# Kernel tuning notes

Hardware: AMD Instinct MI355X
Metric: run time of the kernel (lower is better)

The kernel has to match this reference:

```python
import jax, jax.numpy as jnp
import numpy as np

B, T, D = 32, 1024, 1024
N, L = 77, 768
H = 8
TED = 2048  # time_embed_dim
EPS = 1e-5


def _ln(x, g, b):
    m = jnp.mean(x, axis=-1, keepdims=True)
    v = jnp.var(x, axis=-1, keepdims=True)
    return (x - m) * jax.lax.rsqrt(v + EPS) * g + b


def setup_inputs() -> dict:
    key = jax.random.key(0)
    ks = jax.random.split(key, 16)
    s = lambda fan_in: 1.0 / np.sqrt(fan_in)
    return {
        "x": jax.random.normal(ks[0], (B, T, D), jnp.float32),
        "xf": jax.random.normal(ks[1], (B, N, L), jnp.float32),
        "emb": jax.random.normal(ks[2], (B, TED), jnp.float32),
        "norm_g": jnp.ones((D,), jnp.float32),
        "norm_b": jnp.zeros((D,), jnp.float32),
        "tnorm_g": jnp.ones((L,), jnp.float32),
        "tnorm_b": jnp.zeros((L,), jnp.float32),
        "Wq": jax.random.normal(ks[3], (D, D), jnp.float32) * s(D),
        "bq": jnp.zeros((D,), jnp.float32),
        "Wk": jax.random.normal(ks[4], (L, D), jnp.float32) * s(L),
        "bk": jnp.zeros((D,), jnp.float32),
        "Wv": jax.random.normal(ks[5], (L, D), jnp.float32) * s(L),
        "bv": jnp.zeros((D,), jnp.float32),
        "emb_W": jax.random.normal(ks[6], (TED, 2 * D), jnp.float32) * s(TED),
        "emb_b": jnp.zeros((2 * D,), jnp.float32),
        "onorm_g": jnp.ones((D,), jnp.float32),
        "onorm_b": jnp.zeros((D,), jnp.float32),
        "Wo": jax.random.normal(ks[7], (D, D), jnp.float32) * s(D),
        "bo": jnp.zeros((D,), jnp.float32),
    }


def reference(x, xf, emb, norm_g, norm_b, tnorm_g, tnorm_b, Wq, bq, Wk, bk, Wv, bv,
              emb_W, emb_b, onorm_g, onorm_b, Wo, bo):
    Bc, Tc, Dc = x.shape
    Nc = xf.shape[1]
    hd = Dc // H
    # projections
    q = _ln(x, norm_g, norm_b) @ Wq + bq                      # [B,T,D]
    xfn = _ln(xf, tnorm_g, tnorm_b)                           # [B,N,L]
    k = (xfn @ Wk + bk).reshape(Bc, Nc, H, hd)                # [B,N,H,hd]
    v = (xfn @ Wv + bv).reshape(Bc, Nc, H, hd)                # [B,N,H,hd]
    q = jax.nn.softmax(q.reshape(Bc, Tc, H, hd), axis=-1)     # softmax over head_dim
    k = jax.nn.softmax(k, axis=1)                             # softmax over N (key tokens)
    # linear-attention: no TxN matrix
    attn = jnp.einsum('bnhd,bnhl->bhdl', k, v)                # [B,H,hd,hd]
    y = jnp.einsum('bthd,bhdl->bthl', q, attn).reshape(Bc, Tc, Dc)
    # StylizationBlock
    emb_out = jax.nn.silu(emb) @ emb_W + emb_b                # [B,2D]
    scale, shift = jnp.split(emb_out[:, None, :], 2, axis=2)  # [B,1,D] each
    h = _ln(y, onorm_g, onorm_b) * (1.0 + scale) + shift
    h = jax.nn.silu(h) @ Wo + bo
    return x + h
```

## Files before the change

kernel.cpp:

```cpp
#include <hip/hip_runtime.h>
#include <hip/hip_bf16.h>
#include <math.h>

namespace {

constexpr int Bc  = 32;
constexpr int Tc  = 1024;
constexpr int Dc  = 1024;
constexpr int Nt  = 77;
constexpr int Lc  = 768;
constexpr int HDc = 128;
constexpr int TEDc = 2048;
constexpr float EPSc = 1e-5f;

typedef __attribute__((ext_vector_type(8))) short bf16x8;
typedef __attribute__((ext_vector_type(8))) unsigned short u16x8;
typedef __attribute__((ext_vector_type(4))) float f32x4;

__device__ __forceinline__ float silu_f(float x) { return x / (1.f + __expf(-x)); }

__device__ __forceinline__ unsigned short f2bf(float f) {
  unsigned u = __float_as_uint(f);
  return (unsigned short)((u + 0x7fffu + ((u >> 16) & 1u)) >> 16);
}
__device__ __forceinline__ float bf2f(unsigned short h) {
  return __uint_as_float(((unsigned)h) << 16);
}

__device__ __forceinline__ void gload16(const void* g, void* l) {
  __builtin_amdgcn_global_load_lds((const __attribute__((address_space(1))) void*)g,
                                   (__attribute__((address_space(3))) void*)l, 16, 0, 0);
}

__device__ __forceinline__ int rowswz(int r) {
  return (((r >> 3) & 1) << 1) | ((r >> 1) & 1);
}

__global__ __launch_bounds__(256) void ln_bf16_kernel(
    const float* __restrict__ src, unsigned short* __restrict__ dst, int cols,
    const float* __restrict__ g, const float* __restrict__ b)
{
  const int row = blockIdx.x;
  const float* p = src + (size_t)row * cols;
  const int c = threadIdx.x * 4;
  float4 v = make_float4(0.f, 0.f, 0.f, 0.f);
  if (c < cols) v = *reinterpret_cast<const float4*>(p + c);
  float s  = v.x + v.y + v.z + v.w;
  float sq = v.x * v.x + v.y * v.y + v.z * v.z + v.w * v.w;
  __shared__ float red[2][4];
  __shared__ float mr[2];
  for (int o = 32; o > 0; o >>= 1) { s += __shfl_down(s, o); sq += __shfl_down(sq, o); }
  const int wid = threadIdx.x >> 6, lane = threadIdx.x & 63;
  if (lane == 0) { red[0][wid] = s; red[1][wid] = sq; }
  __syncthreads();
  if (threadIdx.x == 0) {
    const float S  = red[0][0] + red[0][1] + red[0][2] + red[0][3];
    const float SQ = red[1][0] + red[1][1] + red[1][2] + red[1][3];
    const float mean = S / cols;
    const float var  = SQ / cols - mean * mean;
    mr[0] = mean; mr[1] = rsqrtf(var + EPSc);
  }
  __syncthreads();
  if (c < cols) {
    const float mean = mr[0], rstd = mr[1];
    ushort4 o;
    o.x = f2bf((v.x - mean) * rstd * g[c + 0] + b[c + 0]);
    o.y = f2bf((v.y - mean) * rstd * g[c + 1] + b[c + 1]);
    o.z = f2bf((v.z - mean) * rstd * g[c + 2] + b[c + 2]);
    o.w = f2bf((v.w - mean) * rstd * g[c + 3] + b[c + 3]);
    *reinterpret_cast<ushort4*>(dst + (size_t)row * cols + c) = o;
  }
}

__global__ __launch_bounds__(256) void convT_bf16_kernel(
    const float* __restrict__ W, unsigned short* __restrict__ Wt, int K, int N)
{
  __shared__ float t[32][33];
  const int n0 = blockIdx.x * 32, k0 = blockIdx.y * 32;
  const int tx = threadIdx.x & 31, ty = threadIdx.x >> 5;
  #pragma unroll
  for (int dy = 0; dy < 32; dy += 8)
    t[ty + dy][tx] = W[(size_t)(k0 + ty + dy) * N + n0 + tx];
  __syncthreads();
  #pragma unroll
  for (int dy = 0; dy < 32; dy += 8)
    Wt[(size_t)(n0 + ty + dy) * K + k0 + tx] = f2bf(t[tx][ty + dy]);
}

__global__ __launch_bounds__(256) void convT2_bf16_kernel(
    const float* __restrict__ W0, unsigned short* __restrict__ T0,
    const float* __restrict__ W1, unsigned short* __restrict__ T1, int K, int N)
{
  __shared__ float t[32][33];
  const float* W = blockIdx.z ? W1 : W0;
  unsigned short* Wt = blockIdx.z ? T1 : T0;
  const int n0 = blockIdx.x * 32, k0 = blockIdx.y * 32;
  const int tx = threadIdx.x & 31, ty = threadIdx.x >> 5;
  #pragma unroll
  for (int dy = 0; dy < 32; dy += 8)
    t[ty + dy][tx] = W[(size_t)(k0 + ty + dy) * N + n0 + tx];
  __syncthreads();
  #pragma unroll
  for (int dy = 0; dy < 32; dy += 8)
    Wt[(size_t)(n0 + ty + dy) * K + k0 + tx] = f2bf(t[tx][ty + dy]);
}

template<int EPI>
__global__ __launch_bounds__(512) void gemm2_kernel(
    const unsigned short* __restrict__ A, const unsigned short* __restrict__ Bt,
    const float* __restrict__ bias, const float* __restrict__ bias2, int bsplit,
    void* __restrict__ Cout, int M, int K, int N, const float* __restrict__ xres)
{
  constexpr int LDSE = (EPI == 2) ? 32768 : 24576;
  __shared__ unsigned short lds[LDSE];
  const int tid = threadIdx.x, wid = tid >> 6, lane = tid & 63;
  const int ntx = N >> 7;
  int swz = blockIdx.x;
  const int nwg = gridDim.x;
  if ((nwg & 7) == 0) { const int cpx = nwg >> 3; swz = (swz & 7) * cpx + (swz >> 3); }
  const int bx = swz % ntx, by = swz / ntx;
  const int bm0 = by << 8, bn0 = bx << 7;
  const int wr = wid >> 1, wc = wid & 1, lhi = lane >> 4, llo = lane & 15;

  const int srow = lane >> 2;
  const int scol = (((lane & 3) ^ rowswz(srow)) * 8);
  int ar0 = bm0 + wid * 32 + srow;      if (ar0 >= M) ar0 = M - 1;
  int ar1 = bm0 + wid * 32 + 16 + srow; if (ar1 >= M) ar1 = M - 1;
  const int br = bn0 + wid * 16 + srow;
  const unsigned short* Ag0 = A  + (size_t)ar0 * K + scol;
  const unsigned short* Ag1 = A  + (size_t)ar1 * K + scol;
  const unsigned short* Bg  = Bt + (size_t)br  * K + scol;
  const int alc0 = (wid * 2) * 512, alc1 = (wid * 2 + 1) * 512, blc = wid * 512;
  const int rx = rowswz(llo);
  const int aoff = wr * 2048 + llo * 32 + ((lhi ^ rx) * 8);
  const int boff = wc * 2048 + llo * 32 + ((lhi ^ rx) * 8);

  f32x4 acc[4][4] = {};
  const int nt = K >> 5;

  gload16(Ag0, &lds[alc0]);
  gload16(Ag1, &lds[alc1]);
  gload16(Bg,  &lds[16384 + blc]);
  __syncthreads();

  int cur = 0;
  for (int t = 1; t < nt; ++t) {
    const int nb = cur ^ 1;
    const int k0 = t << 5;
    gload16(Ag0 + k0, &lds[nb * 8192 + alc0]);
    gload16(Ag1 + k0, &lds[nb * 8192 + alc1]);
    gload16(Bg  + k0, &lds[16384 + nb * 4096 + blc]);
    bf16x8 a_[4], b_[4];
    #pragma unroll
    for (int mi = 0; mi < 4; mi++) a_[mi] = *(const bf16x8*)(&lds[cur * 8192 + aoff + mi * 512]);
    #pragma unroll
    for (int ni = 0; ni < 4; ni++) b_[ni] = *(const bf16x8*)(&lds[16384 + cur * 4096 + boff + ni * 512]);
    #pragma unroll
    for (int mi = 0; mi < 4; mi++)
      #pragma unroll
      for (int ni = 0; ni < 4; ni++)
        acc[mi][ni] = __builtin_amdgcn_mfma_f32_16x16x32_bf16(a_[mi], b_[ni], acc[mi][ni], 0, 0, 0);
    __syncthreads();
    cur = nb;
  }
  {
    bf16x8 a_[4], b_[4];
    #pragma unroll
    for (int mi = 0; mi < 4; mi++) a_[mi] = *(const bf16x8*)(&lds[cur * 8192 + aoff + mi * 512]);
    #pragma unroll
    for (int ni = 0; ni < 4; ni++) b_[ni] = *(const bf16x8*)(&lds[16384 + cur * 4096 + boff + ni * 512]);
    #pragma unroll
    for (int mi = 0; mi < 4; mi++)
      #pragma unroll
      for (int ni = 0; ni < 4; ni++)
        acc[mi][ni] = __builtin_amdgcn_mfma_f32_16x16x32_bf16(a_[mi], b_[ni], acc[mi][ni], 0, 0, 0);
  }

  if constexpr (EPI != 2) {
    #pragma unroll
    for (int mi = 0; mi < 4; mi++) {
      #pragma unroll
      for (int ni = 0; ni < 4; ni++) {
        const int col = bn0 + wc * 64 + ni * 16 + llo;
        const float bs = (bsplit > 0 && col >= bsplit) ? bias2[col - bsplit] : bias[col];
        #pragma unroll
        for (int r = 0; r < 4; r++) {
          const int row = bm0 + wr * 64 + mi * 16 + lhi * 4 + r;
          if (row < M) {
            float v = acc[mi][ni][r] + bs;
            if (EPI == 1) v += xres[(size_t)row * N + col];
            ((float*)Cout)[(size_t)row * N + col] = v;
          }
        }
      }
    }
  } else {
    __syncthreads();
    #pragma unroll
    for (int mi = 0; mi < 4; mi++) {
      #pragma unroll
      for (int ni = 0; ni < 4; ni++) {
        const int col = wc * 64 + ni * 16 + llo;
        const float bs = bias[bn0 + col];
        #pragma unroll
        for (int r = 0; r < 4; r++) {
          const int row = wr * 64 + mi * 16 + lhi * 4 + r;
          lds[row * 128 + (col ^ ((row & 7) << 3))] = f2bf(acc[mi][ni][r] + bs);
        }
      }
    }
    __syncthreads();
    const int row = tid >> 1, cb = (tid & 1) * 64;
    const int sw = (row & 7) << 3;
    float mx = -1e30f;
    #pragma unroll
    for (int g = 0; g < 8; g++) {
      u16x8 u = *(const u16x8*)(&lds[row * 128 + ((cb + g * 8) ^ sw)]);
      #pragma unroll
      for (int j = 0; j < 8; j++) mx = fmaxf(mx, bf2f(u[j]));
    }
    mx = fmaxf(mx, __shfl_xor(mx, 1));
    float ssum = 0.f;
    #pragma unroll
    for (int g = 0; g < 8; g++) {
      unsigned short* p = &lds[row * 128 + ((cb + g * 8) ^ sw)];
      u16x8 u = *(const u16x8*)p;
      u16x8 e;
      #pragma unroll
      for (int j = 0; j < 8; j++) {
        float ev = __expf(bf2f(u[j]) - mx);
        ssum += ev;
        e[j] = f2bf(ev);
      }
      *(u16x8*)p = e;
    }
    ssum += __shfl_xor(ssum, 1);
    const float inv = 1.f / ssum;
    unsigned short* Cb = (unsigned short*)Cout;
    #pragma unroll
    for (int g = 0; g < 8; g++) {
      u16x8 u = *(const u16x8*)(&lds[row * 128 + ((cb + g * 8) ^ sw)]);
      u16x8 o;
      #pragma unroll
      for (int j = 0; j < 8; j++) o[j] = f2bf(bf2f(u[j]) * inv);
      *(u16x8*)(&Cb[(size_t)(bm0 + row) * N + bn0 + cb + g * 8]) = o;
    }
  }
}

__global__ void softmax_k_kernel(float* __restrict__ kv) {
  const int idx = blockIdx.x * blockDim.x + threadIdx.x;
  const int b = idx >> 10, d = idx & 1023;
  float* p = kv + (size_t)b * Nt * 2048 + d;
  float m = -1e30f;
  for (int n = 0; n < Nt; n++) m = fmaxf(m, p[(size_t)n * 2048]);
  float s = 0.f;
  for (int n = 0; n < Nt; n++) s += __expf(p[(size_t)n * 2048] - m);
  const float inv = 1.f / s;
  for (int n = 0; n < Nt; n++) p[(size_t)n * 2048] = __expf(p[(size_t)n * 2048] - m) * inv;
}

__global__ __launch_bounds__(256) void attn_einsum_kernel(
    const float* __restrict__ kv, unsigned short* __restrict__ attnT) {
  const int bh = blockIdx.x;
  const int b = bh >> 3, h = bh & 7;
  __shared__ float ks[Nt][HDc];
  __shared__ float vs[Nt][HDc];
  const float* kb = kv + (size_t)b * Nt * 2048 + h * HDc;
  const float* vb = kv + (size_t)b * Nt * 2048 + 1024 + h * HDc;
  for (int i = threadIdx.x; i < Nt * HDc; i += 256) {
    const int n = i >> 7, d = i & 127;
    ks[n][d] = kb[(size_t)n * 2048 + d];
    vs[n][d] = vb[(size_t)n * 2048 + d];
  }
  __syncthreads();
  const int tx = threadIdx.x & 15, ty = threadIdx.x >> 4;
  float acc[8][8] = {};
  for (int n = 0; n < Nt; n++) {
    float a[8], w[8];
    #pragma unroll
    for (int i = 0; i < 8; i++) a[i] = vs[n][ty + 16 * i];
    #pragma unroll
    for (int j = 0; j < 8; j++) w[j] = ks[n][tx + 16 * j];
    #pragma unroll
    for (int i = 0; i < 8; i++)
      #pragma unroll
      for (int j = 0; j < 8; j++)
        acc[i][j] += a[i] * w[j];
  }
  unsigned short* ab = attnT + (size_t)bh * HDc * HDc;
  #pragma unroll
  for (int i = 0; i < 8; i++)
    #pragma unroll
    for (int j = 0; j < 8; j++)
      ab[(size_t)(ty + 16 * i) * HDc + tx + 16 * j] = f2bf(acc[i][j]);
}

__global__ __launch_bounds__(256) void y_mfma_kernel(
    unsigned short* __restrict__ q, const unsigned short* __restrict__ attnT)
{
  __shared__ unsigned short lds[16384];
  const int tid = threadIdx.x, wid = tid >> 6, lane = tid & 63;
  const int bh = blockIdx.y, b = bh >> 3, h = bh & 7;
  const int bm0 = blockIdx.x << 7;
  const int wr = wid >> 1, wc = wid & 1, lhi = lane >> 4, llo = lane & 15;

  unsigned short* Abase = q + ((size_t)b * Tc) * Dc + h * HDc;
  const unsigned short* Btb = attnT + (size_t)bh * HDc * HDc;

  const int srow = lane >> 2;
  const int scol = (((lane & 3) ^ rowswz(srow)) * 8);
  const int ar0 = bm0 + wid * 32 + srow, ar1 = ar0 + 16;
  const int br0 = wid * 32 + srow,       br1 = br0 + 16;
  const unsigned short* Ag0 = Abase + (size_t)ar0 * Dc + scol;
  const unsigned short* Ag1 = Abase + (size_t)ar1 * Dc + scol;
  const unsigned short* Bg0 = Btb + (size_t)br0 * HDc + scol;
  const unsigned short* Bg1 = Btb + (size_t)br1 * HDc + scol;
  const int lc0 = (wid * 2 + 0) * 512, lc1 = (wid * 2 + 1) * 512;
  const int rx = rowswz(llo);
  const int aoff = wr * 2048 + llo * 32 + ((lhi ^ rx) * 8);
  const int boff = wc * 2048 + llo * 32 + ((lhi ^ rx) * 8);

  f32x4 acc[4][4] = {};

  gload16(Ag0, &lds[lc0]);
  gload16(Ag1, &lds[lc1]);
  gload16(Bg0, &lds[8192 + lc0]);
  gload16(Bg1, &lds[8192 + lc1]);
  __syncthreads();

  int cur = 0;
  for (int t = 1; t < 4; ++t) {
    const int nb = cur ^ 1;
    const int k0 = t << 5;
    gload16(Ag0 + k0, &lds[nb * 4096 + lc0]);
    gload16(Ag1 + k0, &lds[nb * 4096 + lc1]);
    gload16(Bg0 + k0, &lds[8192 + nb * 4096 + lc0]);
    gload16(Bg1 + k0, &lds[8192 + nb * 4096 + lc1]);
    bf16x8 a_[4], b_[4];
    #pragma unroll
    for (int mi = 0; mi < 4; mi++) a_[mi] = *(const bf16x8*)(&lds[cur * 4096 + aoff + mi * 512]);
    #pragma unroll
    for (int ni = 0; ni < 4; ni++) b_[ni] = *(const bf16x8*)(&lds[8192 + cur * 4096 + boff + ni * 512]);
    #pragma unroll
    for (int mi = 0; mi < 4; mi++)
      #pragma unroll
      for (int ni = 0; ni < 4; ni++)
        acc[mi][ni] = __builtin_amdgcn_mfma_f32_16x16x32_bf16(a_[mi], b_[ni], acc[mi][ni], 0, 0, 0);
    __syncthreads();
    cur = nb;
  }
  {
    bf16x8 a_[4], b_[4];
    #pragma unroll
    for (int mi = 0; mi < 4; mi++) a_[mi] = *(const bf16x8*)(&lds[cur * 4096 + aoff + mi * 512]);
    #pragma unroll
    for (int ni = 0; ni < 4; ni++) b_[ni] = *(const bf16x8*)(&lds[8192 + cur * 4096 + boff + ni * 512]);
    #pragma unroll
    for (int mi = 0; mi < 4; mi++)
      #pragma unroll
      for (int ni = 0; ni < 4; ni++)
        acc[mi][ni] = __builtin_amdgcn_mfma_f32_16x16x32_bf16(a_[mi], b_[ni], acc[mi][ni], 0, 0, 0);
  }

  __syncthreads();
  #pragma unroll
  for (int mi = 0; mi < 4; mi++) {
    #pragma unroll
    for (int ni = 0; ni < 4; ni++) {
      const int col = wc * 64 + ni * 16 + llo;
      #pragma unroll
      for (int r = 0; r < 4; r++) {
        const int row = wr * 64 + mi * 16 + lhi * 4 + r;
        lds[row * 128 + (col ^ ((row & 7) << 3))] = f2bf(acc[mi][ni][r]);
      }
    }
  }
  __syncthreads();
  const int row = tid >> 1, cb = (tid & 1) * 64;
  const int sw = (row & 7) << 3;
  #pragma unroll
  for (int g = 0; g < 8; g++) {
    u16x8 u = *(const u16x8*)(&lds[row * 128 + ((cb + g * 8) ^ sw)]);
    *(u16x8*)(&Abase[(size_t)(bm0 + row) * Dc + cb + g * 8]) = u;
  }
}

__global__ __launch_bounds__(256) void ln_mod_silu_bf16_kernel(
    unsigned short* __restrict__ y, const float* __restrict__ ss,
    const float* __restrict__ g, const float* __restrict__ bvec) {
  const int row = blockIdx.x;
  const int b = row >> 10;
  unsigned short* p = y + (size_t)row * Dc;
  const int c = threadIdx.x * 4;
  ushort4 u = *reinterpret_cast<const ushort4*>(p + c);
  float vv[4] = {bf2f(u.x), bf2f(u.y), bf2f(u.z), bf2f(u.w)};
  float s  = vv[0] + vv[1] + vv[2] + vv[3];
  float sq = vv[0]*vv[0] + vv[1]*vv[1] + vv[2]*vv[2] + vv[3]*vv[3];
  __shared__ float red[2][4];
  __shared__ float mr[2];
  for (int o = 32; o > 0; o >>= 1) { s += __shfl_down(s, o); sq += __shfl_down(sq, o); }
  const int wid = threadIdx.x >> 6, lane = threadIdx.x & 63;
  if (lane == 0) { red[0][wid] = s; red[1][wid] = sq; }
  __syncthreads();
  if (threadIdx.x == 0) {
    const float S  = red[0][0] + red[0][1] + red[0][2] + red[0][3];
    const float SQ = red[1][0] + red[1][1] + red[1][2] + red[1][3];
    const float mean = S / Dc;
    const float var = SQ / Dc - mean * mean;
    mr[0] = mean; mr[1] = rsqrtf(var + EPSc);
  }
  __syncthreads();
  const float mean = mr[0], rstd = mr[1];
  const float* ssb = ss + (size_t)b * 2 * Dc;
  ushort4 o;
  float t0 = (vv[0] - mean) * rstd * g[c + 0] + bvec[c + 0];
  float t1 = (vv[1] - mean) * rstd * g[c + 1] + bvec[c + 1];
  float t2 = (vv[2] - mean) * rstd * g[c + 2] + bvec[c + 2];
  float t3 = (vv[3] - mean) * rstd * g[c + 3] + bvec[c + 3];
  o.x = f2bf(silu_f(t0 * (1.f + ssb[c + 0]) + ssb[Dc + c + 0]));
  o.y = f2bf(silu_f(t1 * (1.f + ssb[c + 1]) + ssb[Dc + c + 1]));
  o.z = f2bf(silu_f(t2 * (1.f + ssb[c + 2]) + ssb[Dc + c + 2]));
  o.w = f2bf(silu_f(t3 * (1.f + ssb[c + 3]) + ssb[Dc + c + 3]));
  *reinterpret_cast<ushort4*>(p + c) = o;
}

__global__ __launch_bounds__(256) void silu_emb_kernel(
    const float* __restrict__ emb, float* __restrict__ sile) {
  const int i = (blockIdx.x * 256 + threadIdx.x) * 4;
  float4 v = *reinterpret_cast<const float4*>(emb + i);
  v.x = silu_f(v.x); v.y = silu_f(v.y); v.z = silu_f(v.z); v.w = silu_f(v.w);
  *reinterpret_cast<float4*>(sile + i) = v;
}

__global__ __launch_bounds__(256) void emb_part_kernel(
    const float* __restrict__ sile, const float* __restrict__ W,
    float* __restrict__ part) {
  const int split = blockIdx.y;
  const int n = blockIdx.x * 256 + threadIdx.x;
  const int k0 = split * 64;
  const float* se = sile + k0;
  const float* Wp = W + (size_t)k0 * (2 * Dc) + n;
  float acc[32] = {};
  for (int kk = 0; kk < 64; kk++) {
    const float w = Wp[(size_t)kk * (2 * Dc)];
    #pragma unroll
    for (int m = 0; m < 32; m++)
      acc[m] = fmaf(se[m * TEDc + kk], w, acc[m]);
  }
  float* pp = part + (size_t)split * 32 * (2 * Dc) + n;
  #pragma unroll
  for (int m = 0; m < 32; m++) pp[(size_t)m * (2 * Dc)] = acc[m];
}

__global__ __launch_bounds__(256) void emb_reduce_kernel(
    const float* __restrict__ part, const float* __restrict__ bias,
    float* __restrict__ ssb) {
  const int i = blockIdx.x * 256 + threadIdx.x;
  const int n = i & (2 * Dc - 1);
  float s = bias[n];
  #pragma unroll 8
  for (int sp = 0; sp < 32; sp++) s += part[(size_t)sp * 32 * (2 * Dc) + i];
  ssb[i] = s;
}

}

extern "C" void kernel_launch(void* const* d_in, const int* in_sizes, int n_in,
                              void* d_out, int out_size, void* d_ws, size_t ws_size,
                              hipStream_t stream) {
  const float* x       = (const float*)d_in[0];
  const float* xf      = (const float*)d_in[1];
  const float* emb     = (const float*)d_in[2];
  const float* norm_g  = (const float*)d_in[3];
  const float* norm_b  = (const float*)d_in[4];
  const float* tnorm_g = (const float*)d_in[5];
  const float* tnorm_b = (const float*)d_in[6];
  const float* Wq      = (const float*)d_in[7];
  const float* bq      = (const float*)d_in[8];
  const float* Wk      = (const float*)d_in[9];
  const float* bk      = (const float*)d_in[10];
  const float* Wv      = (const float*)d_in[11];
  const float* bv_     = (const float*)d_in[12];
  const float* emb_W   = (const float*)d_in[13];
  const float* emb_b   = (const float*)d_in[14];
  const float* onorm_g = (const float*)d_in[15];
  const float* onorm_b = (const float*)d_in[16];
  const float* Wo      = (const float*)d_in[17];
  const float* bo      = (const float*)d_in[18];
  float* out = (float*)d_out;

  char* ws = (char*)d_ws;
  unsigned short* Ab = (unsigned short*)ws;
  char* R = ws;
  unsigned short* qb   = (unsigned short*)(ws + 67108864);
  unsigned short* Wq_t = (unsigned short*)(ws + 134217728);
  unsigned short* Wk_t = (unsigned short*)(ws + 136314880);
  unsigned short* Wv_t = (unsigned short*)(ws + 137887744);
  unsigned short* Wo_t = (unsigned short*)(ws + 139460608);
  float*          ssb  = (float*)(ws + 141557760);
  float*          sile = (float*)(ws + 141819904);
  float*          part = (float*)(ws + 142082048);
  unsigned short* xfb   = (unsigned short*)(R);
  float*          kv    = (float*)(R + 3784704);
  unsigned short* attnT = (unsigned short*)(R + 23969792);

  const int Mq  = Bc * Tc;
  const int Mkv = Bc * Nt;

  ln_bf16_kernel<<<Mq, 256, 0, stream>>>(x, Ab, Dc, norm_g, norm_b);
  convT_bf16_kernel<<<dim3(Dc / 32, Dc / 32), 256, 0, stream>>>(Wq, Wq_t, Dc, Dc);
  convT2_bf16_kernel<<<dim3(Dc / 32, Lc / 32, 2), 256, 0, stream>>>(Wk, Wk_t, Wv, Wv_t, Lc, Dc);
  convT_bf16_kernel<<<dim3(Dc / 32, Dc / 32), 256, 0, stream>>>(Wo, Wo_t, Dc, Dc);

  gemm2_kernel<2><<<(Dc / 128) * (Mq / 256), 512, 0, stream>>>(
      Ab, Wq_t, bq, nullptr, 0, qb, Mq, Dc, Dc, nullptr);

  ln_bf16_kernel<<<Mkv, 256, 0, stream>>>(xf, xfb, Lc, tnorm_g, tnorm_b);
  gemm2_kernel<0><<<(2048 / 128) * ((Mkv + 255) / 256), 512, 0, stream>>>(
      xfb, Wk_t, bk, bv_, 1024, kv, Mkv, Lc, 2048, nullptr);
  softmax_k_kernel<<<(Bc * Dc) / 256, 256, 0, stream>>>(kv);
  attn_einsum_kernel<<<Bc * 8, 256, 0, stream>>>(kv, attnT);

  silu_emb_kernel<<<(Bc * TEDc) / 1024, 256, 0, stream>>>(emb, sile);
  emb_part_kernel<<<dim3(8, 32), 256, 0, stream>>>(sile, emb_W, part);
  emb_reduce_kernel<<<(Bc * 2 * Dc) / 256, 256, 0, stream>>>(part, emb_b, ssb);

  y_mfma_kernel<<<dim3(Tc / 128, Bc * 8), 256, 0, stream>>>(qb, attnT);
  ln_mod_silu_bf16_kernel<<<Mq, 256, 0, stream>>>(qb, ssb, onorm_g, onorm_b);
  gemm2_kernel<1><<<(Dc / 128) * (Mq / 256), 512, 0, stream>>>(
      qb, Wo_t, bo, nullptr, 0, out, Mq, Dc, Dc, x);
}
```

Before: 481.6 us.

## Enlarge GEMM block tile to 256x256 with 2x4 wave layout

```diff
diff --git a/kernel.cpp b/kernel.cpp
--- a/kernel.cpp
+++ b/kernel.cpp
@@ -106,57 +106,60 @@
 }
 
 template<int EPI>
-__global__ __launch_bounds__(512) void gemm2_kernel(
+__global__ __launch_bounds__(512, 2) void gemm2_kernel(
     const unsigned short* __restrict__ A, const unsigned short* __restrict__ Bt,
     const float* __restrict__ bias, const float* __restrict__ bias2, int bsplit,
     void* __restrict__ Cout, int M, int K, int N, const float* __restrict__ xres)
 {
-  constexpr int LDSE = (EPI == 2) ? 32768 : 24576;
-  __shared__ unsigned short lds[LDSE];
+  __shared__ unsigned short lds[32768];
   const int tid = threadIdx.x, wid = tid >> 6, lane = tid & 63;
-  const int ntx = N >> 7;
+  const int ntx = N >> 8;
   int swz = blockIdx.x;
   const int nwg = gridDim.x;
   if ((nwg & 7) == 0) { const int cpx = nwg >> 3; swz = (swz & 7) * cpx + (swz >> 3); }
   const int bx = swz % ntx, by = swz / ntx;
-  const int bm0 = by << 8, bn0 = bx << 7;
-  const int wr = wid >> 1, wc = wid & 1, lhi = lane >> 4, llo = lane & 15;
+  const int bm0 = by << 8, bn0 = bx << 8;
+  const int wr = wid >> 2, wc = wid & 3, lhi = lane >> 4, llo = lane & 15;
 
   const int srow = lane >> 2;
   const int scol = (((lane & 3) ^ rowswz(srow)) * 8);
   int ar0 = bm0 + wid * 32 + srow;      if (ar0 >= M) ar0 = M - 1;
   int ar1 = bm0 + wid * 32 + 16 + srow; if (ar1 >= M) ar1 = M - 1;
-  const int br = bn0 + wid * 16 + srow;
+  const int br0 = bn0 + wid * 32 + srow;
+  const int br1 = br0 + 16;
   const unsigned short* Ag0 = A  + (size_t)ar0 * K + scol;
   const unsigned short* Ag1 = A  + (size_t)ar1 * K + scol;
-  const unsigned short* Bg  = Bt + (size_t)br  * K + scol;
-  const int alc0 = (wid * 2) * 512, alc1 = (wid * 2 + 1) * 512, blc = wid * 512;
+  const unsigned short* Bg0 = Bt + (size_t)br0 * K + scol;
+  const unsigned short* Bg1 = Bt + (size_t)br1 * K + scol;
+  const int lc0 = (wid * 2) * 512, lc1 = (wid * 2 + 1) * 512;
   const int rx = rowswz(llo);
-  const int aoff = wr * 2048 + llo * 32 + ((lhi ^ rx) * 8);
-  const int boff = wc * 2048 + llo * 32 + ((lhi ^ rx) * 8);
-
-  f32x4 acc[4][4] = {};
+  const int aoff = wr * 8 * 512 + llo * 32 + ((lhi ^ rx) * 8);
+  const int boff = wc * 4 * 512 + llo * 32 + ((lhi ^ rx) * 8);
+
+  f32x4 acc[8][4] = {};
   const int nt = K >> 5;
 
-  gload16(Ag0, &lds[alc0]);
-  gload16(Ag1, &lds[alc1]);
-  gload16(Bg,  &lds[16384 + blc]);
+  gload16(Ag0, &lds[lc0]);
+  gload16(Ag1, &lds[lc1]);
+  gload16(Bg0, &lds[16384 + lc0]);
+  gload16(Bg1, &lds[16384 + lc1]);
   __syncthreads();
 
   int cur = 0;
   for (int t = 1; t < nt; ++t) {
     const int nb = cur ^ 1;
     const int k0 = t << 5;
-    gload16(Ag0 + k0, &lds[nb * 8192 + alc0]);
-    gload16(Ag1 + k0, &lds[nb * 8192 + alc1]);
-    gload16(Bg  + k0, &lds[16384 + nb * 4096 + blc]);
-    bf16x8 a_[4], b_[4];
-    #pragma unroll
-    for (int mi = 0; mi < 4; mi++) a_[mi] = *(const bf16x8*)(&lds[cur * 8192 + aoff + mi * 512]);
-    #pragma unroll
-    for (int ni = 0; ni < 4; ni++) b_[ni] = *(const bf16x8*)(&lds[16384 + cur * 4096 + boff + ni * 512]);
-    #pragma unroll
-    for (int mi = 0; mi < 4; mi++)
+    gload16(Ag0 + k0, &lds[nb * 8192 + lc0]);
+    gload16(Ag1 + k0, &lds[nb * 8192 + lc1]);
+    gload16(Bg0 + k0, &lds[16384 + nb * 8192 + lc0]);
+    gload16(Bg1 + k0, &lds[16384 + nb * 8192 + lc1]);
+    bf16x8 a_[8], b_[4];
+    #pragma unroll
+    for (int mi = 0; mi < 8; mi++) a_[mi] = *(const bf16x8*)(&lds[cur * 8192 + aoff + mi * 512]);
+    #pragma unroll
+    for (int ni = 0; ni < 4; ni++) b_[ni] = *(const bf16x8*)(&lds[16384 + cur * 8192 + boff + ni * 512]);
+    #pragma unroll
+    for (int mi = 0; mi < 8; mi++)
       #pragma unroll
       for (int ni = 0; ni < 4; ni++)
         acc[mi][ni] = __builtin_amdgcn_mfma_f32_16x16x32_bf16(a_[mi], b_[ni], acc[mi][ni], 0, 0, 0);
@@ -164,13 +167,13 @@
     cur = nb;
   }
   {
-    bf16x8 a_[4], b_[4];
-    #pragma unroll
-    for (int mi = 0; mi < 4; mi++) a_[mi] = *(const bf16x8*)(&lds[cur * 8192 + aoff + mi * 512]);
-    #pragma unroll
-    for (int ni = 0; ni < 4; ni++) b_[ni] = *(const bf16x8*)(&lds[16384 + cur * 4096 + boff + ni * 512]);
-    #pragma unroll
-    for (int mi = 0; mi < 4; mi++)
+    bf16x8 a_[8], b_[4];
+    #pragma unroll
+    for (int mi = 0; mi < 8; mi++) a_[mi] = *(const bf16x8*)(&lds[cur * 8192 + aoff + mi * 512]);
+    #pragma unroll
+    for (int ni = 0; ni < 4; ni++) b_[ni] = *(const bf16x8*)(&lds[16384 + cur * 8192 + boff + ni * 512]);
+    #pragma unroll
+    for (int mi = 0; mi < 8; mi++)
       #pragma unroll
       for (int ni = 0; ni < 4; ni++)
         acc[mi][ni] = __builtin_amdgcn_mfma_f32_16x16x32_bf16(a_[mi], b_[ni], acc[mi][ni], 0, 0, 0);
@@ -178,14 +181,14 @@
 
   if constexpr (EPI != 2) {
     #pragma unroll
-    for (int mi = 0; mi < 4; mi++) {
+    for (int mi = 0; mi < 8; mi++) {
       #pragma unroll
       for (int ni = 0; ni < 4; ni++) {
         const int col = bn0 + wc * 64 + ni * 16 + llo;
         const float bs = (bsplit > 0 && col >= bsplit) ? bias2[col - bsplit] : bias[col];
         #pragma unroll
         for (int r = 0; r < 4; r++) {
-          const int row = bm0 + wr * 64 + mi * 16 + lhi * 4 + r;
+          const int row = bm0 + wr * 128 + mi * 16 + lhi * 4 + r;
           if (row < M) {
             float v = acc[mi][ni][r] + bs;
             if (EPI == 1) v += xres[(size_t)row * N + col];
@@ -195,55 +198,54 @@
       }
     }
   } else {
+    unsigned short* Cb = (unsigned short*)Cout;
     __syncthreads();
     #pragma unroll
-    for (int mi = 0; mi < 4; mi++) {
-      #pragma unroll
-      for (int ni = 0; ni < 4; ni++) {
-        const int col = wc * 64 + ni * 16 + llo;
-        const float bs = bias[bn0 + col];
+    for (int h = 0; h < 2; ++h) {
+      if ((wc >> 1) == h) {
         #pragma unroll
-        for (int r = 0; r < 4; r++) {
-          const int row = wr * 64 + mi * 16 + lhi * 4 + r;
-          lds[row * 128 + (col ^ ((row & 7) << 3))] = f2bf(acc[mi][ni][r] + bs);
+        for (int mi = 0; mi < 8; mi++) {
+          #pragma unroll
+          for (int ni = 0; ni < 4; ni++) {
+            const int lcol = (wc & 1) * 64 + ni * 16 + llo;
+            const float bs = bias[bn0 + h * 128 + lcol];
+            #pragma unroll
+            for (int r = 0; r < 4; r++) {
+              const int lrow = wr * 128 + mi * 16 + lhi * 4 + r;
+              lds[lrow * 128 + (lcol ^ ((lrow & 7) << 3))] = f2bf(acc[mi][ni][r] + bs);
+            }
+          }
         }
       }
-    }
-    __syncthreads();
-    const int row = tid >> 1, cb = (tid & 1) * 64;
-    const int sw = (row & 7) << 3;
-    float mx = -1e30f;
-    #pragma unroll
-    for (int g = 0; g < 8; g++) {
-      u16x8 u = *(const u16x8*)(&lds[row * 128 + ((cb + g * 8) ^ sw)]);
-      #pragma unroll
-      for (int j = 0; j < 8; j++) mx = fmaxf(mx, bf2f(u[j]));
-    }
-    mx = fmaxf(mx, __shfl_xor(mx, 1));
-    float ssum = 0.f;
-    #pragma unroll
-    for (int g = 0; g < 8; g++) {
-      unsigned short* p = &lds[row * 128 + ((cb + g * 8) ^ sw)];
-      u16x8 u = *(const u16x8*)p;
-      u16x8 e;
-      #pragma unroll
-      for (int j = 0; j < 8; j++) {
-        float ev = __expf(bf2f(u[j]) - mx);
-        ssum += ev;
-        e[j] = f2bf(ev);
+      __syncthreads();
+      const int row = tid >> 1, cb = (tid & 1) * 64;
+      const int sw = (row & 7) << 3;
+      float mx = -1e30f;
+      #pragma unroll
+      for (int g = 0; g < 8; g++) {
+        u16x8 u = *(const u16x8*)(&lds[row * 128 + ((cb + g * 8) ^ sw)]);
+        #pragma unroll
+        for (int j = 0; j < 8; j++) mx = fmaxf(mx, bf2f(u[j]));
       }
-      *(u16x8*)p = e;
-    }
-    ssum += __shfl_xor(ssum, 1);
-    const float inv = 1.f / ssum;
-    unsigned short* Cb = (unsigned short*)Cout;
-    #pragma unroll
-    for (int g = 0; g < 8; g++) {
-      u16x8 u = *(const u16x8*)(&lds[row * 128 + ((cb + g * 8) ^ sw)]);
-      u16x8 o;
-      #pragma unroll
-      for (int j = 0; j < 8; j++) o[j] = f2bf(bf2f(u[j]) * inv);
-      *(u16x8*)(&Cb[(size_t)(bm0 + row) * N + bn0 + cb + g * 8]) = o;
+      mx = fmaxf(mx, __shfl_xor(mx, 1));
+      float ssum = 0.f;
+      float ev[8][8];
+      #pragma unroll
+      for (int g = 0; g < 8; g++) {
+        u16x8 u = *(const u16x8*)(&lds[row * 128 + ((cb + g * 8) ^ sw)]);
+        #pragma unroll
+        for (int j = 0; j < 8; j++) { ev[g][j] = __expf(bf2f(u[j]) - mx); ssum += ev[g][j]; }
+      }
+      ssum += __shfl_xor(ssum, 1);
+      const float inv = 1.f / ssum;
+      #pragma unroll
+      for (int g = 0; g < 8; g++) {
+        u16x8 o;
+        #pragma unroll
+        for (int j = 0; j < 8; j++) o[j] = f2bf(ev[g][j] * inv);
+        *(u16x8*)(&Cb[(size_t)(bm0 + row) * N + bn0 + h * 128 + cb + g * 8]) = o;
+      }
+      __syncthreads();
     }
   }
 }
@@ -513,11 +515,11 @@
   convT2_bf16_kernel<<<dim3(Dc / 32, Lc / 32, 2), 256, 0, stream>>>(Wk, Wk_t, Wv, Wv_t, Lc, Dc);
   convT_bf16_kernel<<<dim3(Dc / 32, Dc / 32), 256, 0, stream>>>(Wo, Wo_t, Dc, Dc);
 
-  gemm2_kernel<2><<<(Dc / 128) * (Mq / 256), 512, 0, stream>>>(
+  gemm2_kernel<2><<<(Dc / 256) * (Mq / 256), 512, 0, stream>>>(
       Ab, Wq_t, bq, nullptr, 0, qb, Mq, Dc, Dc, nullptr);
 
   ln_bf16_kernel<<<Mkv, 256, 0, stream>>>(xf, xfb, Lc, tnorm_g, tnorm_b);
-  gemm2_kernel<0><<<(2048 / 128) * ((Mkv + 255) / 256), 512, 0, stream>>>(
+  gemm2_kernel<0><<<(2048 / 256) * ((Mkv + 255) / 256), 512, 0, stream>>>(
       xfb, Wk_t, bk, bv_, 1024, kv, Mkv, Lc, 2048, nullptr);
   softmax_k_kernel<<<(Bc * Dc) / 256, 256, 0, stream>>>(kv);
   attn_einsum_kernel<<<Bc * 8, 256, 0, stream>>>(kv, attnT);
@@ -528,6 +530,6 @@
 
   y_mfma_kernel<<<dim3(Tc / 128, Bc * 8), 256, 0, stream>>>(qb, attnT);
   ln_mod_silu_bf16_kernel<<<Mq, 256, 0, stream>>>(qb, ssb, onorm_g, onorm_b);
-  gemm2_kernel<1><<<(Dc / 128) * (Mq / 256), 512, 0, stream>>>(
+  gemm2_kernel<1><<<(Dc / 256) * (Mq / 256), 512, 0, stream>>>(
       qb, Wo_t, bo, nullptr, 0, out, Mq, Dc, Dc, x);
 }
```

Result: slower. 524.5 us (+8.9%).

## Fuse key softmax into attention einsum kernel and drop LDS swizzle

Applied to the files above, without the earlier changes.

```diff
diff --git a/kernel.cpp b/kernel.cpp
--- a/kernel.cpp
+++ b/kernel.cpp
@@ -30,10 +30,6 @@
 __device__ __forceinline__ void gload16(const void* g, void* l) {
   __builtin_amdgcn_global_load_lds((const __attribute__((address_space(1))) void*)g,
                                    (__attribute__((address_space(3))) void*)l, 16, 0, 0);
-}
-
-__device__ __forceinline__ int rowswz(int r) {
-  return (((r >> 3) & 1) << 1) | ((r >> 1) & 1);
 }
 
 __global__ __launch_bounds__(256) void ln_bf16_kernel(
@@ -122,8 +118,7 @@
   const int bm0 = by << 8, bn0 = bx << 7;
   const int wr = wid >> 1, wc = wid & 1, lhi = lane >> 4, llo = lane & 15;
 
-  const int srow = lane >> 2;
-  const int scol = (((lane & 3) ^ rowswz(srow)) * 8);
+  const int srow = lane >> 2, scol = (lane & 3) * 8;
   int ar0 = bm0 + wid * 32 + srow;      if (ar0 >= M) ar0 = M - 1;
   int ar1 = bm0 + wid * 32 + 16 + srow; if (ar1 >= M) ar1 = M - 1;
   const int br = bn0 + wid * 16 + srow;
@@ -131,9 +126,8 @@
   const unsigned short* Ag1 = A  + (size_t)ar1 * K + scol;
   const unsigned short* Bg  = Bt + (size_t)br  * K + scol;
   const int alc0 = (wid * 2) * 512, alc1 = (wid * 2 + 1) * 512, blc = wid * 512;
-  const int rx = rowswz(llo);
-  const int aoff = wr * 2048 + llo * 32 + ((lhi ^ rx) * 8);
-  const int boff = wc * 2048 + llo * 32 + ((lhi ^ rx) * 8);
+  const int aoff = wr * 2048 + llo * 32 + lhi * 8;
+  const int boff = wc * 2048 + llo * 32 + lhi * 8;
 
   f32x4 acc[4][4] = {};
   const int nt = K >> 5;
@@ -248,19 +242,7 @@
   }
 }
 
-__global__ void softmax_k_kernel(float* __restrict__ kv) {
-  const int idx = blockIdx.x * blockDim.x + threadIdx.x;
-  const int b = idx >> 10, d = idx & 1023;
-  float* p = kv + (size_t)b * Nt * 2048 + d;
-  float m = -1e30f;
-  for (int n = 0; n < Nt; n++) m = fmaxf(m, p[(size_t)n * 2048]);
-  float s = 0.f;
-  for (int n = 0; n < Nt; n++) s += __expf(p[(size_t)n * 2048] - m);
-  const float inv = 1.f / s;
-  for (int n = 0; n < Nt; n++) p[(size_t)n * 2048] = __expf(p[(size_t)n * 2048] - m) * inv;
-}
-
-__global__ __launch_bounds__(256) void attn_einsum_kernel(
+__global__ __launch_bounds__(256) void attn_fused_kernel(
     const float* __restrict__ kv, unsigned short* __restrict__ attnT) {
   const int bh = blockIdx.x;
   const int b = bh >> 3, h = bh & 7;
@@ -274,6 +256,16 @@
     vs[n][d] = vb[(size_t)n * 2048 + d];
   }
   __syncthreads();
+  if (threadIdx.x < HDc) {
+    const int d = threadIdx.x;
+    float m = -1e30f;
+    for (int n = 0; n < Nt; n++) m = fmaxf(m, ks[n][d]);
+    float s = 0.f;
+    for (int n = 0; n < Nt; n++) { float e = __expf(ks[n][d] - m); ks[n][d] = e; s += e; }
+    const float inv = 1.f / s;
+    for (int n = 0; n < Nt; n++) ks[n][d] *= inv;
+  }
+  __syncthreads();
   const int tx = threadIdx.x & 15, ty = threadIdx.x >> 4;
   float acc[8][8] = {};
   for (int n = 0; n < Nt; n++) {
@@ -308,8 +300,7 @@
   unsigned short* Abase = q + ((size_t)b * Tc) * Dc + h * HDc;
   const unsigned short* Btb = attnT + (size_t)bh * HDc * HDc;
 
-  const int srow = lane >> 2;
-  const int scol = (((lane & 3) ^ rowswz(srow)) * 8);
+  const int srow = lane >> 2, scol = (lane & 3) * 8;
   const int ar0 = bm0 + wid * 32 + srow, ar1 = ar0 + 16;
   const int br0 = wid * 32 + srow,       br1 = br0 + 16;
   const unsigned short* Ag0 = Abase + (size_t)ar0 * Dc + scol;
@@ -317,9 +308,8 @@
   const unsigned short* Bg0 = Btb + (size_t)br0 * HDc + scol;
   const unsigned short* Bg1 = Btb + (size_t)br1 * HDc + scol;
   const int lc0 = (wid * 2 + 0) * 512, lc1 = (wid * 2 + 1) * 512;
-  const int rx = rowswz(llo);
-  const int aoff = wr * 2048 + llo * 32 + ((lhi ^ rx) * 8);
-  const int boff = wc * 2048 + llo * 32 + ((lhi ^ rx) * 8);
+  const int aoff = wr * 2048 + llo * 32 + lhi * 8;
+  const int boff = wc * 2048 + llo * 32 + lhi * 8;
 
   f32x4 acc[4][4] = {};
 
@@ -519,8 +509,7 @@
   ln_bf16_kernel<<<Mkv, 256, 0, stream>>>(xf, xfb, Lc, tnorm_g, tnorm_b);
   gemm2_kernel<0><<<(2048 / 128) * ((Mkv + 255) / 256), 512, 0, stream>>>(
       xfb, Wk_t, bk, bv_, 1024, kv, Mkv, Lc, 2048, nullptr);
-  softmax_k_kernel<<<(Bc * Dc) / 256, 256, 0, stream>>>(kv);
-  attn_einsum_kernel<<<Bc * 8, 256, 0, stream>>>(kv, attnT);
+  attn_fused_kernel<<<Bc * 8, 256, 0, stream>>>(kv, attnT);
 
   silu_emb_kernel<<<(Bc * TEDc) / 1024, 256, 0, stream>>>(emb, sile);
   emb_part_kernel<<<dim3(8, 32), 256, 0, stream>>>(sile, emb_W, part);
```

Result: faster. 461.0 us (-4.3%).
